# Kernel optimization log

Measured on AMD Instinct MI355X. Metric: run time of the kernel, lower is better.

The kernel has to match this reference:

```python
import jax, jax.numpy as jnp
import numpy as np

# MORRConfig_20um_MQ (all-pass MRR) constants used by mrr_roundtrip_phase_to_tr(intensity=True)
A = 0.987   # attenuation_factor a
R = 0.99    # coupling_factor r
KS, STRIDE, PAD = 3, 1, 1
IN_C, OUT_C, MB = 32, 64, 8


def _unfold(x, ks, pad, stride):
    # torch.nn.functional.unfold: output channel order is (C, kh, kw), C slowest
    B, C, H, W = x.shape
    xp = jnp.pad(x, ((0, 0), (0, 0), (pad, pad), (pad, pad)))
    Ho = (H + 2 * pad - ks) // stride + 1
    Wo = (W + 2 * pad - ks) // stride + 1
    cols = jnp.stack(
        [xp[:, :, i:i + stride * Ho:stride, j:j + stride * Wo:stride]
         for i in range(ks) for j in range(ks)],
        axis=2,
    )  # [B, C, ks*ks, Ho, Wo]
    return cols.reshape(B, C * ks * ks, Ho * Wo), Ho, Wo


def _mrr_tr(phase):
    # all-pass MRR intensity transmission vs roundtrip phase detuning
    c = jnp.cos(phase)
    return (A * A - 2.0 * A * R * c + R * R) / (1.0 - 2.0 * A * R * c + (A * R) ** 2)


def setup_inputs() -> dict:
    key = jax.random.key(0)
    k1, k2, k3 = jax.random.split(key, 3)
    B, H, W = 8, 64, 64
    wic = IN_C * KS * KS           # 288, divisible by miniblock -> no zero pad
    q = wic // MB                  # grid_dim_x = 36
    p = OUT_C // MB                # grid_dim_y = 8
    x = jax.random.normal(k1, (B, IN_C, H, W), jnp.float32)
    weight = jax.random.normal(k2, (p, q, MB), jnp.float32)
    morr_output_scale = jax.random.normal(k3, (max(1, q // 2) + 1,), jnp.float32)
    return {"x": x, "weight": weight, "morr_output_scale": morr_output_scale}


def reference(x, weight, morr_output_scale):
    B = x.shape[0]
    p, q, k = weight.shape
    w = jnp.abs(weight)                                  # w_bit=16 -> build_weight() = |W|
    cols, Ho, Wo = _unfold(x, KS, PAD, STRIDE)           # [B, wic, L]
    xf = cols.transpose(0, 2, 1).reshape(-1, q, k)       # [N, q, k], N = B*Ho*Wo
    xf = xf * xf                                         # intensity modulation x^2
    # block-circulant matvec via rFFT (circular convolution per (p, q) block)
    Xf = jnp.fft.rfft(xf, n=k, axis=-1)                  # [N, q, kf]
    Wf = jnp.fft.rfft(w, n=k, axis=-1)                   # [p, q, kf]
    phase = jnp.fft.irfft(Xf[:, None, :, :] * Wf[None, :, :, :], n=k, axis=-1)  # [N, p, q, k]
    tr = _mrr_tr(phase)                                  # MORR nonlinear transfer
    # differential-rail output scale (even grid_dim_x branch)
    s = morr_output_scale
    if q % 2 == 0:
        scale = jnp.concatenate([s[:-1], -s[:-1]])
    else:
        scale = jnp.concatenate([s[:-1], s[-1:], -s[:-1]])
    out = jnp.einsum('npqk,q->npk', tr, scale).reshape(-1, p * k)[:, :OUT_C]
    return out.reshape(B, Ho, Wo, OUT_C).transpose(0, 3, 1, 2)  # [B, OUT_C, Ho, Wo]
```

## Files before the change

kernel.cpp:

```cpp
#include <hip/hip_runtime.h>
#include <math.h>
#include <utility>


template <class F, size_t... I>
__device__ __forceinline__ void sf_impl(F&& f, std::index_sequence<I...>) {
    (f(std::integral_constant<size_t, I>{}), ...);
}
template <size_t N, class F>
__device__ __forceinline__ void static_for(F&& f) {
    sf_impl(f, std::make_index_sequence<N>{});
}

__global__ __launch_bounds__(1024, 8)
void morr_kernel(const float* __restrict__ xg, const float* __restrict__ wg,
                 const float* __restrict__ sg, float* __restrict__ out) {
    __shared__ union {
        float x[32 * 10 * 40];
        float ex[2][4][8][64];
    } sm;

    constexpr double Ad = 0.987, Rd = 0.99;
    constexpr float K2 = (float)(2.0 * Ad * Rd);
    constexpr float C2 = (float)(1.0 + (Ad * Rd) * (Ad * Rd));
    constexpr float D  = (float)((1.0 - Ad * Ad) * (1.0 - Rd * Rd));
    constexpr float INV2PI = 0.15915494309189535f;

    const int tid = threadIdx.x;
    const int b   = blockIdx.z;
    const int gr0 = blockIdx.y * 8;
    const int gc0 = blockIdx.x * 8;

    for (int i = tid; i < 3200; i += 1024) {
        int c = i / 100, rem = i - c * 100;
        int r = rem / 10, cl = rem - r * 10;
        int gr = gr0 - 1 + r, gc = gc0 - 1 + cl;
        float v = 0.f;
        if ((unsigned)gr < 64u && (unsigned)gc < 64u)
            v = xg[((b * 32 + c) * 64 + gr) * 64 + gc];
        sm.x[c * 400 + r * 40 + cl] = v * v * INV2PI;
    }
    __syncthreads();

    const int px  = tid & 63;
    const int qhu = __builtin_amdgcn_readfirstlane((tid >> 6) & 1);
    const int p   = __builtin_amdgcn_readfirstlane(tid >> 7);
    const int row = px >> 3;
    const int col = px & 7;

    const float* __restrict__ xb = &sm.x[row * 40 + col];
    const unsigned* __restrict__ wp =
        reinterpret_cast<const unsigned*>(wg) + p * 288 + qhu * 144;
    const unsigned* __restrict__ sp = reinterpret_cast<const unsigned*>(sg);
    const unsigned sgnbit = ((unsigned)qhu) << 31;

    float acc[8];
    static_for<8>([&](auto T) { acc[T] = 0.f; });

    static_for<2>([&](auto CBL) {
        constexpr int cbl = CBL;
        const float* __restrict__ xcb = xb + (qhu * 2 + cbl) * 3200;
        static_for<9>([&](auto QQ) {
            constexpr int qq = QQ;
            float xq[8];
            static_for<8>([&](auto S) {
                constexpr int s   = S;
                constexpr int u   = qq * 8 + s;
                constexpr int off = (u / 9) * 400 + ((u % 9) / 3) * 40 + (u % 3);
                xq[s] = xcb[off];
            });
            float wv[8];
            static_for<8>([&](auto J) {
                constexpr int j = J;
                wv[j] = __uint_as_float(wp[cbl * 72 + qq * 8 + j] & 0x7fffffffu);
            });
            const float sv = __uint_as_float(sp[cbl * 9 + qq] ^ sgnbit);

            static_for<8>([&](auto T) {
                constexpr int t = T;
                float ph = xq[0] * wv[t];
                static_for<7>([&](auto S) {
                    constexpr int s = (int)S + 1;
                    ph = fmaf(xq[s], wv[(t - s + 8) & 7], ph);
                });
                float cv  = __builtin_amdgcn_cosf(ph);
                float den = fmaf(-K2, cv, C2);
                float inv = __builtin_amdgcn_rcpf(den);
                acc[t] = fmaf(sv, inv, acc[t]);
            });
        });
    });

    __syncthreads();
    if (qhu == 0) {
        static_for<4>([&](auto J) { sm.ex[0][J][p][px] = acc[4 + (int)J]; });
    } else {
        static_for<4>([&](auto J) { sm.ex[1][J][p][px] = acc[(int)J]; });
    }
    __syncthreads();

    const int gr = gr0 + row, gc = gc0 + col;
    if (qhu == 0) {
        static_for<4>([&](auto J) {
            constexpr int j = J;
            float v = acc[j] + sm.ex[1][j][p][px];
            out[((b * 64 + p * 8 + j) * 64 + gr) * 64 + gc] = -D * v;
        });
    } else {
        static_for<4>([&](auto J) {
            constexpr int j = J;
            float v = acc[4 + j] + sm.ex[0][j][p][px];
            out[((b * 64 + p * 8 + 4 + j) * 64 + gr) * 64 + gc] = -D * v;
        });
    }
}

extern "C" void kernel_launch(void* const* d_in, const int* in_sizes, int n_in,
                              void* d_out, int out_size, void* d_ws, size_t ws_size,
                              hipStream_t stream) {
    const float* x = (const float*)d_in[0];
    const float* w = (const float*)d_in[1];
    const float* s = (const float*)d_in[2];
    float* out = (float*)d_out;
    dim3 grid(8, 8, 8);
    dim3 block(1024);
    hipLaunchKernelGGL(morr_kernel, grid, block, 0, stream, x, w, s, out);
}
```

Measured before the change: 93.65 us.

## Pair differential-rail q blocks algebraically and split outputs across half-warps

Each thread now handles the matching q and q+18 blocks together, since their scales are s and -s. The two transmission terms are combined as (c1-c2)/(den1*den2), which needs one reciprocal instead of two. Output channels are split by halves between the two thread groups, so the shared-memory exchange and its extra barriers go away. Each thread still does the same number of cosines and FMAs. Folding the difference algebraically may slightly change floating-point rounding.

```diff
diff --git a/kernel.cpp b/kernel.cpp
--- a/kernel.cpp
+++ b/kernel.cpp
@@ -15,15 +15,12 @@
 __global__ __launch_bounds__(1024, 8)
 void morr_kernel(const float* __restrict__ xg, const float* __restrict__ wg,
                  const float* __restrict__ sg, float* __restrict__ out) {
-    __shared__ union {
-        float x[32 * 10 * 40];
-        float ex[2][4][8][64];
-    } sm;
+    __shared__ __align__(16) float smx[32 * 10 * 40];
 
     constexpr double Ad = 0.987, Rd = 0.99;
-    constexpr float K2 = (float)(2.0 * Ad * Rd);
-    constexpr float C2 = (float)(1.0 + (Ad * Rd) * (Ad * Rd));
-    constexpr float D  = (float)((1.0 - Ad * Ad) * (1.0 - Rd * Rd));
+    constexpr float K2  = (float)(2.0 * Ad * Rd);
+    constexpr float C2  = (float)(1.0 + (Ad * Rd) * (Ad * Rd));
+    constexpr float NDK = (float)(-(1.0 - Ad * Ad) * (1.0 - Rd * Rd) * (2.0 * Ad * Rd));
     constexpr float INV2PI = 0.15915494309189535f;
 
     const int tid = threadIdx.x;
@@ -38,81 +35,65 @@
         float v = 0.f;
         if ((unsigned)gr < 64u && (unsigned)gc < 64u)
             v = xg[((b * 32 + c) * 64 + gr) * 64 + gc];
-        sm.x[c * 400 + r * 40 + cl] = v * v * INV2PI;
+        smx[c * 400 + r * 40 + cl] = v * v * INV2PI;
     }
     __syncthreads();
 
     const int px  = tid & 63;
-    const int qhu = __builtin_amdgcn_readfirstlane((tid >> 6) & 1);
+    const int th4 = __builtin_amdgcn_readfirstlane(((tid >> 6) & 1) * 4);
     const int p   = __builtin_amdgcn_readfirstlane(tid >> 7);
     const int row = px >> 3;
     const int col = px & 7;
 
-    const float* __restrict__ xb = &sm.x[row * 40 + col];
-    const unsigned* __restrict__ wp =
-        reinterpret_cast<const unsigned*>(wg) + p * 288 + qhu * 144;
-    const unsigned* __restrict__ sp = reinterpret_cast<const unsigned*>(sg);
-    const unsigned sgnbit = ((unsigned)qhu) << 31;
+    const float* __restrict__ xb = &smx[row * 40 + col];
+    const unsigned* __restrict__ wgu =
+        reinterpret_cast<const unsigned*>(wg) + p * 288;
 
-    float acc[8];
-    static_for<8>([&](auto T) { acc[T] = 0.f; });
+    float acc[4];
+    static_for<4>([&](auto J) { acc[J] = 0.f; });
 
-    static_for<2>([&](auto CBL) {
-        constexpr int cbl = CBL;
-        const float* __restrict__ xcb = xb + (qhu * 2 + cbl) * 3200;
-        static_for<9>([&](auto QQ) {
-            constexpr int qq = QQ;
-            float xq[8];
-            static_for<8>([&](auto S) {
-                constexpr int s   = S;
-                constexpr int u   = qq * 8 + s;
-                constexpr int off = (u / 9) * 400 + ((u % 9) / 3) * 40 + (u % 3);
-                xq[s] = xcb[off];
+    static_for<18>([&](auto QP) {
+        constexpr int qp = QP;
+        float xl[8], xh[8];
+        static_for<8>([&](auto S) {
+            constexpr int s   = S;
+            constexpr int u   = qp * 8 + s;
+            constexpr int off = (u / 9) * 400 + ((u % 9) / 3) * 40 + (u % 3);
+            xl[s] = xb[off];
+            xh[s] = xb[off + 6400];
+        });
+        float wl[8], wh[8];
+        static_for<8>([&](auto Jw) {
+            constexpr int j = Jw;
+            wl[j] = __uint_as_float(wgu[qp * 8 + (j ^ th4)] & 0x7fffffffu);
+            wh[j] = __uint_as_float(wgu[144 + qp * 8 + (j ^ th4)] & 0x7fffffffu);
+        });
+        const float sv = sg[qp];
+
+        static_for<4>([&](auto J) {
+            constexpr int t = J;
+            float p1 = xl[0] * wl[t];
+            float p2 = xh[0] * wh[t];
+            static_for<7>([&](auto S) {
+                constexpr int s = (int)S + 1;
+                p1 = fmaf(xl[s], wl[(t - s + 8) & 7], p1);
+                p2 = fmaf(xh[s], wh[(t - s + 8) & 7], p2);
             });
-            float wv[8];
-            static_for<8>([&](auto J) {
-                constexpr int j = J;
-                wv[j] = __uint_as_float(wp[cbl * 72 + qq * 8 + j] & 0x7fffffffu);
-            });
-            const float sv = __uint_as_float(sp[cbl * 9 + qq] ^ sgnbit);
-
-            static_for<8>([&](auto T) {
-                constexpr int t = T;
-                float ph = xq[0] * wv[t];
-                static_for<7>([&](auto S) {
-                    constexpr int s = (int)S + 1;
-                    ph = fmaf(xq[s], wv[(t - s + 8) & 7], ph);
-                });
-                float cv  = __builtin_amdgcn_cosf(ph);
-                float den = fmaf(-K2, cv, C2);
-                float inv = __builtin_amdgcn_rcpf(den);
-                acc[t] = fmaf(sv, inv, acc[t]);
-            });
+            float c1 = __builtin_amdgcn_cosf(p1);
+            float c2 = __builtin_amdgcn_cosf(p2);
+            float a  = fmaf(-K2, c1, C2);
+            float bb = fmaf(-K2, c2, C2);
+            float rr = __builtin_amdgcn_rcpf(a * bb);
+            acc[J] = fmaf(sv, (c1 - c2) * rr, acc[J]);
         });
     });
 
-    __syncthreads();
-    if (qhu == 0) {
-        static_for<4>([&](auto J) { sm.ex[0][J][p][px] = acc[4 + (int)J]; });
-    } else {
-        static_for<4>([&](auto J) { sm.ex[1][J][p][px] = acc[(int)J]; });
-    }
-    __syncthreads();
-
     const int gr = gr0 + row, gc = gc0 + col;
-    if (qhu == 0) {
-        static_for<4>([&](auto J) {
-            constexpr int j = J;
-            float v = acc[j] + sm.ex[1][j][p][px];
-            out[((b * 64 + p * 8 + j) * 64 + gr) * 64 + gc] = -D * v;
-        });
-    } else {
-        static_for<4>([&](auto J) {
-            constexpr int j = J;
-            float v = acc[4 + j] + sm.ex[0][j][p][px];
-            out[((b * 64 + p * 8 + 4 + j) * 64 + gr) * 64 + gc] = -D * v;
-        });
-    }
+    static_for<4>([&](auto J) {
+        constexpr int j = J;
+        const int oc = p * 8 + th4 + j;
+        out[((b * 64 + oc) * 64 + gr) * 64 + gc] = NDK * acc[j];
+    });
 }
 
 extern "C" void kernel_launch(void* const* d_in, const int* in_sizes, int n_in,
```

Result: no change. 92.18 us (-1.6%).
